# Kernel tuning notes

Hardware: AMD Instinct MI355X
Metric: run time of the kernel (lower is better)

## Reference

```python
import jax, jax.numpy as jnp
import numpy as np


def setup_inputs() -> dict:
    key = jax.random.key(0)
    ks = jax.random.split(key, 9)
    bs, F, T, d_in, Nh, d_out = 4, 8, 256, 64, 8, 64
    std = 2.0  # gaussian_init_delta_std
    return {
        "X": jax.random.normal(ks[0], (bs, F, T, d_in), dtype=jnp.float32),
        "attention_center": std * jax.random.normal(ks[1], (F, Nh, 1), dtype=jnp.float32),
        "alpha": jax.random.normal(ks[2], (F,), dtype=jnp.float32),
        "W_query": jax.random.normal(ks[3], (F, T, d_in, Nh, 2), dtype=jnp.float32),
        "W_key": jax.random.normal(ks[4], (F, T, d_in, Nh, 2), dtype=jnp.float32),
        "Wkey_": jax.random.normal(ks[5], (F, 2, 2), dtype=jnp.float32),
        "u": jax.random.normal(ks[6], (F, T, 2), dtype=jnp.float32),
        "W": jax.random.normal(ks[7], (F, Nh * d_in, d_out), dtype=jnp.float32),
        "b": jax.random.normal(ks[8], (F, T, d_out), dtype=jnp.float32),
    }


def reference(X, attention_center, alpha, W_query, W_key, Wkey_, u, W, b):
    bs, F, T, d_in = X.shape
    Nh = W_query.shape[3]

    # relative-position features R[t,l] = (l-t)^2, (l-t); identical across F in the original
    rel = (jnp.arange(T)[None, :] - jnp.arange(T)[:, None]).astype(jnp.float32)
    R = jnp.stack([rel ** 2, rel], axis=-1)  # (T,T,2)

    query = jnp.einsum('bftd,ftdhe->bfthe', X, W_query)  # (bs,F,T,Nh,2)
    key = jnp.einsum('bftd,ftdhe->bfthe', X, W_key)      # (bs,F,T,Nh,2)

    r_delta = jnp.einsum('fde,tle->ftld', Wkey_, R)      # (F,T,T,2)

    centers = jnp.concatenate([jnp.ones_like(attention_center), -2.0 * attention_center], axis=-1)  # (F,Nh,2)
    v = -alpha[:, None, None] * centers                  # (F,Nh,2)

    scores = (
        jnp.einsum('bfthe,bflhe->bfthl', query, key)
        + jnp.einsum('bfthe,ftle->bfthl', query, r_delta)
        + jnp.einsum('fle,bfthe->bfthl', u, key)
        + jnp.einsum('fhe,ftle->fthl', v, r_delta)[None]
    )  # (bs,F,T,Nh,T)

    probs = jax.nn.softmax(scores, axis=-1)

    vals = jnp.einsum('bfthl,bfld->bfthd', probs, X)     # (bs,F,T,Nh,d_in)
    vals = vals.reshape(bs, F, T, Nh * d_in)

    return jnp.einsum('bftd,fdo->bfto', vals, W) + b     # (bs,F,T,d_out)
```

## Files before the change

kernel.cpp:

```cpp
#include <hip/hip_runtime.h>
#include <hip/hip_bf16.h>

#define BS 4
#define NF 8
#define NT 256
#define DIN 64
#define NH 8
#define DOUT 64
#define TT 4
#define MROWS 32
#define NCH 64

typedef unsigned short u16;
typedef __attribute__((ext_vector_type(8))) short short8;
typedef __attribute__((ext_vector_type(4))) float f32x4;
typedef __attribute__((ext_vector_type(4))) unsigned int u32x4;

static __device__ __forceinline__ u16 f2bf(float x) {
    __hip_bfloat16 h = __float2bfloat16(x);
    u16 r; __builtin_memcpy(&r, &h, 2); return r;
}
static __device__ __forceinline__ unsigned pk2(float a, float b) {
    return (unsigned)f2bf(a) | ((unsigned)f2bf(b) << 16);
}

__global__ __launch_bounds__(256) void prep_kernel(
    const float* __restrict__ X,
    const float* __restrict__ Wq,
    const float* __restrict__ Wk,
    const float* __restrict__ W,
    float* __restrict__ q,
    float* __restrict__ kT,
    u16* __restrict__ XT,
    u16* __restrict__ Wt)
{
    __shared__ float sm[4160];
    const int tid = threadIdx.x;
    const int bid = blockIdx.x;

    if (bid < 2048) {
        const int ft = bid;
        const int f = ft >> 8, t = ft & 255;
        float* sWt = sm;
        float* sX  = sm + 2176;

        float4 a4 = ((const float4*)(Wq + ((size_t)ft << 10)))[tid];
        float4 b4 = ((const float4*)(Wk + ((size_t)ft << 10)))[tid];
        {
            int d = tid >> 2, he = (tid & 3) << 2;
            sWt[(he + 0) * 68 + d] = a4.x;
            sWt[(he + 1) * 68 + d] = a4.y;
            sWt[(he + 2) * 68 + d] = a4.z;
            sWt[(he + 3) * 68 + d] = a4.w;
            sWt[1088 + (he + 0) * 68 + d] = b4.x;
            sWt[1088 + (he + 1) * 68 + d] = b4.y;
            sWt[1088 + (he + 2) * 68 + d] = b4.z;
            sWt[1088 + (he + 3) * 68 + d] = b4.w;
            int xb = tid >> 6, xd = tid & 63;
            sX[tid] = X[(((size_t)((xb * NF + f) * NT + t)) << 6) + xd];
        }
        __syncthreads();

        const int half  = tid & 1;
        const int he    = (tid >> 1) & 15;
        const int b     = (tid >> 5) & 3;
        const int which = tid >> 7;
        const float* wp = sWt + which * 1088 + he * 68 + (half << 5);
        const float* xp = sX + (b << 6) + (half << 5);
        float acc = 0.f;
        #pragma unroll
        for (int j = 0; j < 8; ++j) {
            float4 w = *(const float4*)(wp + (j << 2));
            float4 x = *(const float4*)(xp + (j << 2));
            acc = fmaf(w.x, x.x, acc);
            acc = fmaf(w.y, x.y, acc);
            acc = fmaf(w.z, x.z, acc);
            acc = fmaf(w.w, x.w, acc);
        }
        acc += __shfl_xor(acc, 1);
        if (half == 0) {
            int bf = b * NF + f;
            if (which) kT[(((size_t)(bf * 16 + he)) << 8) + t] = acc;
            else       q[(((size_t)(bf * NT + t)) << 4) + he] = acc;
        }
    } else if (bid < 2176) {
        const int idx = bid - 2048;
        const int bf = idx >> 2, lc = idx & 3;
        float (*sT)[65] = (float(*)[65])sm;
        #pragma unroll
        for (int i = 0; i < 16; ++i) {
            int l = i * 4 + (tid >> 6), d = tid & 63;
            sT[l][d] = X[(((size_t)(bf * NT) + lc * 64 + l) << 6) + d];
        }
        __syncthreads();
        #pragma unroll
        for (int i = 0; i < 16; ++i) {
            int d = i * 4 + (tid >> 6), l = tid & 63;
            XT[(((size_t)(bf * 64) + d) << 8) + lc * 64 + l] = f2bf(sT[l][d]);
        }
    } else {
        const int idx = bid - 2176;
        const int f = idx >> 3, kc = idx & 7;
        float (*sT)[65] = (float(*)[65])sm;
        #pragma unroll
        for (int i = 0; i < 16; ++i) {
            int kk = i * 4 + (tid >> 6), o = tid & 63;
            sT[kk][o] = W[(((size_t)(f * 512) + kc * 64 + kk) << 6) + o];
        }
        __syncthreads();
        #pragma unroll
        for (int i = 0; i < 16; ++i) {
            int o = i * 4 + (tid >> 6), kk = tid & 63;
            Wt[(((size_t)(f * 64) + o) << 9) + kc * 64 + kk] = f2bf(sT[kk][o]);
        }
    }
}

__global__ __launch_bounds__(256, 4) void attn_kernel(
    const float* __restrict__ ac,
    const float* __restrict__ alpha,
    const float* __restrict__ Wkey_,
    const float* __restrict__ u,
    const float* __restrict__ bias,
    const float* __restrict__ q,
    const float* __restrict__ kT,
    const u16* __restrict__ XT,
    const u16* __restrict__ Wt,
    float* __restrict__ out)
{
    __shared__ __align__(16) u16 sPV[8320];
    __shared__ float sRed[MROWS * 16];
    __shared__ float sM[MROWS];
    __shared__ float sInvS[MROWS];

    const int tid = threadIdx.x;
    const int bid = blockIdx.x;
    const int ch = bid & 63;
    const int f  = (bid >> 6) & 7;
    const int b  = bid >> 9;
    const int bf = b * NF + f;
    const int t0 = ch * TT;

    const int h  = tid & 7;
    const int tp = (tid >> 3) & 1;
    const int lg = tid >> 4;
    const int t_a = t0 + tp * 2, t_b = t_a + 1;
    const int m_a = tp * 16 + h, m_b = m_a + 8;
    const int lbase = lg * 16;

    const float* kT0 = kT + ((size_t)bf << 12) + ((h * 2) << 8);
    const float* kT1 = kT0 + 256;
    const float* up  = u + (f << 9);

    float q0a, q1a, kt0a, kt1a, c2a, c1a;
    float q0b, q1b, kt0b, kt1b, c2b, c1b;
    {
        float al = alpha[f];
        float acv = ac[f * 8 + h];
        float wk0 = Wkey_[f * 4],     wk1 = Wkey_[f * 4 + 1];
        float wk2 = Wkey_[f * 4 + 2], wk3 = Wkey_[f * 4 + 3];
        float2 qa = *(const float2*)(q + ((size_t)(bf * NT + t_a) << 4) + (h << 1));
        float2 qb = *(const float2*)(q + ((size_t)(bf * NT + t_b) << 4) + (h << 1));
        q0a = qa.x; q1a = qa.y; q0b = qb.x; q1b = qb.y;
        kt0a = kT0[t_a]; kt1a = kT1[t_a];
        kt0b = kT0[t_b]; kt1b = kT1[t_b];
        float a0 = q0a - al, a1 = q1a + 2.f * al * acv;
        c2a = a0 * wk0 + a1 * wk2; c1a = a0 * wk1 + a1 * wk3;
        a0 = q0b - al; a1 = q1b + 2.f * al * acv;
        c2b = a0 * wk0 + a1 * wk2; c1b = a0 * wk1 + a1 * wk3;
    }

    float sA[16], sB[16];
    float mxa = -1e30f, mxb = -1e30f;
    #pragma unroll
    for (int g = 0; g < 4; ++g) {
        const int l0 = lbase + g * 4;
        float4 K0 = *(const float4*)(kT0 + l0);
        float4 K1 = *(const float4*)(kT1 + l0);
        float4 U0 = *(const float4*)(up + (l0 << 1));
        float4 U1 = *(const float4*)(up + (l0 << 1) + 4);
        float k0s[4] = {K0.x, K0.y, K0.z, K0.w};
        float k1s[4] = {K1.x, K1.y, K1.z, K1.w};
        float u0s[4] = {U0.x, U0.z, U1.x, U1.z};
        float u1s[4] = {U0.y, U0.w, U1.y, U1.w};
        #pragma unroll
        for (int j = 0; j < 4; ++j) {
            float rela = (float)(l0 + j - t_a);
            float relb = rela - 1.f;
            float sa = (c2a * rela + c1a) * rela;
            sa = fmaf(q0a, k0s[j], sa); sa = fmaf(q1a, k1s[j], sa);
            sa = fmaf(kt0a, u0s[j], sa); sa = fmaf(kt1a, u1s[j], sa);
            float sb = (c2b * relb + c1b) * relb;
            sb = fmaf(q0b, k0s[j], sb); sb = fmaf(q1b, k1s[j], sb);
            sb = fmaf(kt0b, u0s[j], sb); sb = fmaf(kt1b, u1s[j], sb);
            sA[g * 4 + j] = sa; sB[g * 4 + j] = sb;
            mxa = fmaxf(mxa, sa); mxb = fmaxf(mxb, sb);
        }
    }
    sRed[m_a * 16 + lg] = mxa;
    sRed[m_b * 16 + lg] = mxb;
    __syncthreads();
    if (tid < MROWS) {
        const float4* r4 = (const float4*)(sRed + tid * 16);
        float4 r0 = r4[0], r1 = r4[1], r2 = r4[2], r3 = r4[3];
        float mm = fmaxf(fmaxf(fmaxf(r0.x, r0.y), fmaxf(r0.z, r0.w)),
                         fmaxf(fmaxf(r1.x, r1.y), fmaxf(r1.z, r1.w)));
        mm = fmaxf(mm, fmaxf(fmaxf(fmaxf(r2.x, r2.y), fmaxf(r2.z, r2.w)),
                             fmaxf(fmaxf(r3.x, r3.y), fmaxf(r3.z, r3.w))));
        sM[tid] = mm;
    }
    __syncthreads();

    u16* sP = sPV;
    {
        const float Ma = sM[m_a], Mb = sM[m_b];
        float suma = 0.f, sumb = 0.f;
        unsigned pka[4], pkb[4];
        float epa = 0.f, epb = 0.f;
        #pragma unroll
        for (int j = 0; j < 16; ++j) {
            float ea = __expf(sA[j] - Ma), eb = __expf(sB[j] - Mb);
            suma += ea; sumb += eb;
            if ((j & 1) == 0) { epa = ea; epb = eb; }
            else { pka[(j & 7) >> 1] = pk2(epa, ea); pkb[(j & 7) >> 1] = pk2(epb, eb); }
            if ((j & 7) == 7) {
                int chunk = lg * 2 + (j >> 3);
                int pa = chunk ^ h;
                int pb = chunk ^ (h + 8);
                *(u32x4*)&sP[m_a * 256 + pa * 8] = (u32x4){pka[0], pka[1], pka[2], pka[3]};
                *(u32x4*)&sP[m_b * 256 + pb * 8] = (u32x4){pkb[0], pkb[1], pkb[2], pkb[3]};
            }
        }
        sRed[m_a * 16 + lg] = suma;
        sRed[m_b * 16 + lg] = sumb;
    }

    const int wv   = tid >> 6;
    const int lane = tid & 63;
    const int quad = lane >> 4;
    const int ln   = lane & 15;
    const int mh   = wv & 1;
    const int nh   = wv >> 1;
    const u16* xb = XT + ((size_t)bf << 14);
    short8 nb0, nb1;
    {
        int l2 = quad * 8;
        nb0 = *(const short8*)(xb + (nh * 32 + ln) * 256 + l2);
        nb1 = *(const short8*)(xb + (nh * 32 + 16 + ln) * 256 + l2);
    }
    __syncthreads();
    if (tid < MROWS) {
        const float4* r4 = (const float4*)(sRed + tid * 16);
        float4 r0 = r4[0], r1 = r4[1], r2 = r4[2], r3 = r4[3];
        float ss = ((r0.x + r0.y) + (r0.z + r0.w)) + ((r1.x + r1.y) + (r1.z + r1.w))
                 + ((r2.x + r2.y) + (r2.z + r2.w)) + ((r3.x + r3.y) + (r3.z + r3.w));
        sInvS[tid] = 1.f / ss;
    }
    __syncthreads();

    f32x4 acc0 = {0.f, 0.f, 0.f, 0.f}, acc1 = acc0;
    #pragma unroll
    for (int ks = 0; ks < 8; ++ks) {
        short8 b0 = nb0, b1 = nb1;
        if (ks < 7) {
            int l2 = (ks + 1) * 32 + quad * 8;
            nb0 = *(const short8*)(xb + (nh * 32 + ln) * 256 + l2);
            nb1 = *(const short8*)(xb + (nh * 32 + 16 + ln) * 256 + l2);
        }
        int phys = (ks * 4 + quad) ^ ln;
        short8 a = *(const short8*)&sP[(mh * 16 + ln) * 256 + phys * 8];
        acc0 = __builtin_amdgcn_mfma_f32_16x16x32_bf16(a, b0, acc0, 0, 0, 0);
        acc1 = __builtin_amdgcn_mfma_f32_16x16x32_bf16(a, b1, acc1, 0, 0, 0);
    }
    float inv0 = sInvS[mh * 16 + quad * 4 + 0];
    float inv1 = sInvS[mh * 16 + quad * 4 + 1];
    float inv2 = sInvS[mh * 16 + quad * 4 + 2];
    float inv3 = sInvS[mh * 16 + quad * 4 + 3];
    const u16* wb = Wt + ((size_t)(f * 64 + wv * 16 + ln) << 9);
    short8 nw = *(const short8*)(wb + quad * 8);
    __syncthreads();

    u16* sVals = sPV;
    {
        float invs[4] = {inv0, inv1, inv2, inv3};
        #pragma unroll
        for (int reg = 0; reg < 4; ++reg) {
            int mg = mh * 16 + quad * 4 + reg;
            int tl = mg >> 3, hh = mg & 7;
            u16* dst = sVals + tl * 520 + hh * 64 + nh * 32 + ln;
            dst[0]  = f2bf(acc0[reg] * invs[reg]);
            dst[16] = f2bf(acc1[reg] * invs[reg]);
        }
    }
    __syncthreads();

    f32x4 oacc = {0.f, 0.f, 0.f, 0.f};
    #pragma unroll
    for (int ks = 0; ks < 16; ++ks) {
        short8 bw = nw;
        if (ks < 15) nw = *(const short8*)(wb + (ks + 1) * 32 + quad * 8);
        short8 a = *(const short8*)(sVals + ln * 520 + ks * 32 + quad * 8);
        oacc = __builtin_amdgcn_mfma_f32_16x16x32_bf16(a, bw, oacc, 0, 0, 0);
    }
    {
        int o = wv * 16 + ln;
        #pragma unroll
        for (int reg = 0; reg < 4; ++reg) {
            int tl = quad * 4 + reg;
            if (tl < TT) {
                int tg = t0 + tl;
                out[((size_t)(bf * NT + tg) << 6) + o] =
                    oacc[reg] + bias[((size_t)(f * NT + tg) << 6) + o];
            }
        }
    }
}

extern "C" void kernel_launch(void* const* d_in, const int* in_sizes, int n_in,
                              void* d_out, int out_size, void* d_ws, size_t ws_size,
                              hipStream_t stream) {
    const float* X     = (const float*)d_in[0];
    const float* ac    = (const float*)d_in[1];
    const float* alpha = (const float*)d_in[2];
    const float* Wq    = (const float*)d_in[3];
    const float* Wk    = (const float*)d_in[4];
    const float* Wkey_ = (const float*)d_in[5];
    const float* u     = (const float*)d_in[6];
    const float* W     = (const float*)d_in[7];
    const float* bb    = (const float*)d_in[8];
    float* out = (float*)d_out;

    float* qws = (float*)d_ws;
    float* kTp = qws + 131072;
    u16* XT = (u16*)(kTp + 131072);
    u16* Wt = XT + 524288;

    hipLaunchKernelGGL(prep_kernel, dim3(2240), dim3(256), 0, stream,
                       X, Wq, Wk, W, qws, kTp, XT, Wt);
    hipLaunchKernelGGL(attn_kernel, dim3(BS * NF * NCH), dim3(256), 0, stream,
                       ac, alpha, Wkey_, u, bb, qws, kTp, XT, Wt, out);
}
```

Before: 125.5 us.

## Use wave-local shuffle softmax reductions instead of shared-memory block reductions

Remaps the score computation so each wavefront owns one query time step, with each lane covering 32 keys for one head. The row max and sum are then reduced with cross-lane shuffles instead of shared-memory staging, which removes three block-wide barriers and the sRed/sM arrays. The XT prefetch for the first MFMA step is also issued earlier, before the score computation. In exchange, each thread holds 32 score registers, which may raise register pressure under the launch bound.

```diff
diff --git a/kernel.cpp b/kernel.cpp
--- a/kernel.cpp
+++ b/kernel.cpp
@@ -129,8 +129,6 @@
     float* __restrict__ out)
 {
     __shared__ __align__(16) u16 sPV[8320];
-    __shared__ float sRed[MROWS * 16];
-    __shared__ float sM[MROWS];
     __shared__ float sInvS[MROWS];
 
     const int tid = threadIdx.x;
@@ -141,121 +139,93 @@
     const int bf = b * NF + f;
     const int t0 = ch * TT;
 
-    const int h  = tid & 7;
-    const int tp = (tid >> 3) & 1;
-    const int lg = tid >> 4;
-    const int t_a = t0 + tp * 2, t_b = t_a + 1;
-    const int m_a = tp * 16 + h, m_b = m_a + 8;
-    const int lbase = lg * 16;
+    const int w    = tid >> 6;
+    const int lane = tid & 63;
+    const int h    = lane & 7;
+    const int lg   = lane >> 3;
+    const int t    = t0 + w;
+    const int m    = w * 8 + h;
+    const int l0   = lg * 32;
+
+    const int quad = lane >> 4;
+    const int ln   = lane & 15;
+    const int mh   = w & 1;
+    const int nh2  = w >> 1;
+
+    const u16* xb = XT + ((size_t)bf << 14);
+    short8 nb0 = *(const short8*)(xb + (nh2 * 32 + ln) * 256 + quad * 8);
+    short8 nb1 = *(const short8*)(xb + (nh2 * 32 + 16 + ln) * 256 + quad * 8);
 
     const float* kT0 = kT + ((size_t)bf << 12) + ((h * 2) << 8);
     const float* kT1 = kT0 + 256;
     const float* up  = u + (f << 9);
 
-    float q0a, q1a, kt0a, kt1a, c2a, c1a;
-    float q0b, q1b, kt0b, kt1b, c2b, c1b;
+    float q0, q1, kt0, kt1, c2, c1;
     {
         float al = alpha[f];
         float acv = ac[f * 8 + h];
         float wk0 = Wkey_[f * 4],     wk1 = Wkey_[f * 4 + 1];
         float wk2 = Wkey_[f * 4 + 2], wk3 = Wkey_[f * 4 + 3];
-        float2 qa = *(const float2*)(q + ((size_t)(bf * NT + t_a) << 4) + (h << 1));
-        float2 qb = *(const float2*)(q + ((size_t)(bf * NT + t_b) << 4) + (h << 1));
-        q0a = qa.x; q1a = qa.y; q0b = qb.x; q1b = qb.y;
-        kt0a = kT0[t_a]; kt1a = kT1[t_a];
-        kt0b = kT0[t_b]; kt1b = kT1[t_b];
-        float a0 = q0a - al, a1 = q1a + 2.f * al * acv;
-        c2a = a0 * wk0 + a1 * wk2; c1a = a0 * wk1 + a1 * wk3;
-        a0 = q0b - al; a1 = q1b + 2.f * al * acv;
-        c2b = a0 * wk0 + a1 * wk2; c1b = a0 * wk1 + a1 * wk3;
-    }
-
-    float sA[16], sB[16];
-    float mxa = -1e30f, mxb = -1e30f;
+        float2 qv = *(const float2*)(q + ((size_t)(bf * NT + t) << 4) + (h << 1));
+        q0 = qv.x; q1 = qv.y;
+        kt0 = kT0[t]; kt1 = kT1[t];
+        float a0 = q0 - al, a1 = q1 + 2.f * al * acv;
+        c2 = a0 * wk0 + a1 * wk2; c1 = a0 * wk1 + a1 * wk3;
+    }
+
+    float s[32];
+    float mx = -1e30f;
     #pragma unroll
     for (int g = 0; g < 4; ++g) {
-        const int l0 = lbase + g * 4;
-        float4 K0 = *(const float4*)(kT0 + l0);
-        float4 K1 = *(const float4*)(kT1 + l0);
-        float4 U0 = *(const float4*)(up + (l0 << 1));
-        float4 U1 = *(const float4*)(up + (l0 << 1) + 4);
-        float k0s[4] = {K0.x, K0.y, K0.z, K0.w};
-        float k1s[4] = {K1.x, K1.y, K1.z, K1.w};
-        float u0s[4] = {U0.x, U0.z, U1.x, U1.z};
-        float u1s[4] = {U0.y, U0.w, U1.y, U1.w};
-        #pragma unroll
-        for (int j = 0; j < 4; ++j) {
-            float rela = (float)(l0 + j - t_a);
-            float relb = rela - 1.f;
-            float sa = (c2a * rela + c1a) * rela;
-            sa = fmaf(q0a, k0s[j], sa); sa = fmaf(q1a, k1s[j], sa);
-            sa = fmaf(kt0a, u0s[j], sa); sa = fmaf(kt1a, u1s[j], sa);
-            float sb = (c2b * relb + c1b) * relb;
-            sb = fmaf(q0b, k0s[j], sb); sb = fmaf(q1b, k1s[j], sb);
-            sb = fmaf(kt0b, u0s[j], sb); sb = fmaf(kt1b, u1s[j], sb);
-            sA[g * 4 + j] = sa; sB[g * 4 + j] = sb;
-            mxa = fmaxf(mxa, sa); mxb = fmaxf(mxb, sb);
-        }
-    }
-    sRed[m_a * 16 + lg] = mxa;
-    sRed[m_b * 16 + lg] = mxb;
-    __syncthreads();
-    if (tid < MROWS) {
-        const float4* r4 = (const float4*)(sRed + tid * 16);
-        float4 r0 = r4[0], r1 = r4[1], r2 = r4[2], r3 = r4[3];
-        float mm = fmaxf(fmaxf(fmaxf(r0.x, r0.y), fmaxf(r0.z, r0.w)),
-                         fmaxf(fmaxf(r1.x, r1.y), fmaxf(r1.z, r1.w)));
-        mm = fmaxf(mm, fmaxf(fmaxf(fmaxf(r2.x, r2.y), fmaxf(r2.z, r2.w)),
-                             fmaxf(fmaxf(r3.x, r3.y), fmaxf(r3.z, r3.w))));
-        sM[tid] = mm;
-    }
-    __syncthreads();
+        const int lb = l0 + g * 8;
+        float4 K0a = *(const float4*)(kT0 + lb);
+        float4 K0b = *(const float4*)(kT0 + lb + 4);
+        float4 K1a = *(const float4*)(kT1 + lb);
+        float4 K1b = *(const float4*)(kT1 + lb + 4);
+        float4 Ua = *(const float4*)(up + (lb << 1));
+        float4 Ub = *(const float4*)(up + (lb << 1) + 4);
+        float4 Uc = *(const float4*)(up + (lb << 1) + 8);
+        float4 Ud = *(const float4*)(up + (lb << 1) + 12);
+        float k0[8] = {K0a.x, K0a.y, K0a.z, K0a.w, K0b.x, K0b.y, K0b.z, K0b.w};
+        float k1[8] = {K1a.x, K1a.y, K1a.z, K1a.w, K1b.x, K1b.y, K1b.z, K1b.w};
+        float u0[8] = {Ua.x, Ua.z, Ub.x, Ub.z, Uc.x, Uc.z, Ud.x, Ud.z};
+        float u1[8] = {Ua.y, Ua.w, Ub.y, Ub.w, Uc.y, Uc.w, Ud.y, Ud.w};
+        #pragma unroll
+        for (int j = 0; j < 8; ++j) {
+            float rel = (float)(lb + j - t);
+            float sv = (c2 * rel + c1) * rel;
+            sv = fmaf(q0, k0[j], sv);
+            sv = fmaf(q1, k1[j], sv);
+            sv = fmaf(kt0, u0[j], sv);
+            sv = fmaf(kt1, u1[j], sv);
+            s[g * 8 + j] = sv;
+            mx = fmaxf(mx, sv);
+        }
+    }
+    mx = fmaxf(mx, __shfl_xor(mx, 8));
+    mx = fmaxf(mx, __shfl_xor(mx, 16));
+    mx = fmaxf(mx, __shfl_xor(mx, 32));
 
     u16* sP = sPV;
-    {
-        const float Ma = sM[m_a], Mb = sM[m_b];
-        float suma = 0.f, sumb = 0.f;
-        unsigned pka[4], pkb[4];
-        float epa = 0.f, epb = 0.f;
-        #pragma unroll
-        for (int j = 0; j < 16; ++j) {
-            float ea = __expf(sA[j] - Ma), eb = __expf(sB[j] - Mb);
-            suma += ea; sumb += eb;
-            if ((j & 1) == 0) { epa = ea; epb = eb; }
-            else { pka[(j & 7) >> 1] = pk2(epa, ea); pkb[(j & 7) >> 1] = pk2(epb, eb); }
-            if ((j & 7) == 7) {
-                int chunk = lg * 2 + (j >> 3);
-                int pa = chunk ^ h;
-                int pb = chunk ^ (h + 8);
-                *(u32x4*)&sP[m_a * 256 + pa * 8] = (u32x4){pka[0], pka[1], pka[2], pka[3]};
-                *(u32x4*)&sP[m_b * 256 + pb * 8] = (u32x4){pkb[0], pkb[1], pkb[2], pkb[3]};
-            }
-        }
-        sRed[m_a * 16 + lg] = suma;
-        sRed[m_b * 16 + lg] = sumb;
-    }
-
-    const int wv   = tid >> 6;
-    const int lane = tid & 63;
-    const int quad = lane >> 4;
-    const int ln   = lane & 15;
-    const int mh   = wv & 1;
-    const int nh   = wv >> 1;
-    const u16* xb = XT + ((size_t)bf << 14);
-    short8 nb0, nb1;
-    {
-        int l2 = quad * 8;
-        nb0 = *(const short8*)(xb + (nh * 32 + ln) * 256 + l2);
-        nb1 = *(const short8*)(xb + (nh * 32 + 16 + ln) * 256 + l2);
-    }
-    __syncthreads();
-    if (tid < MROWS) {
-        const float4* r4 = (const float4*)(sRed + tid * 16);
-        float4 r0 = r4[0], r1 = r4[1], r2 = r4[2], r3 = r4[3];
-        float ss = ((r0.x + r0.y) + (r0.z + r0.w)) + ((r1.x + r1.y) + (r1.z + r1.w))
-                 + ((r2.x + r2.y) + (r2.z + r2.w)) + ((r3.x + r3.y) + (r3.z + r3.w));
-        sInvS[tid] = 1.f / ss;
-    }
+    float sum = 0.f;
+    #pragma unroll
+    for (int c = 0; c < 4; ++c) {
+        unsigned pk4[4];
+        #pragma unroll
+        for (int jj = 0; jj < 8; jj += 2) {
+            float e0 = __expf(s[c * 8 + jj] - mx);
+            float e1 = __expf(s[c * 8 + jj + 1] - mx);
+            sum += e0 + e1;
+            pk4[jj >> 1] = pk2(e0, e1);
+        }
+        int chunk = lg * 4 + c;
+        int phys = chunk ^ (m & 15);
+        *(u32x4*)&sP[m * 256 + phys * 8] = (u32x4){pk4[0], pk4[1], pk4[2], pk4[3]};
+    }
+    sum += __shfl_xor(sum, 8);
+    sum += __shfl_xor(sum, 16);
+    sum += __shfl_xor(sum, 32);
+    if (lg == 0) sInvS[m] = 1.f / sum;
     __syncthreads();
 
     f32x4 acc0 = {0.f, 0.f, 0.f, 0.f}, acc1 = acc0;
@@ -264,8 +234,8 @@
         short8 b0 = nb0, b1 = nb1;
         if (ks < 7) {
             int l2 = (ks + 1) * 32 + quad * 8;
-            nb0 = *(const short8*)(xb + (nh * 32 + ln) * 256 + l2);
-            nb1 = *(const short8*)(xb + (nh * 32 + 16 + ln) * 256 + l2);
+            nb0 = *(const short8*)(xb + (nh2 * 32 + ln) * 256 + l2);
+            nb1 = *(const short8*)(xb + (nh2 * 32 + 16 + ln) * 256 + l2);
         }
         int phys = (ks * 4 + quad) ^ ln;
         short8 a = *(const short8*)&sP[(mh * 16 + ln) * 256 + phys * 8];
@@ -276,7 +246,7 @@
     float inv1 = sInvS[mh * 16 + quad * 4 + 1];
     float inv2 = sInvS[mh * 16 + quad * 4 + 2];
     float inv3 = sInvS[mh * 16 + quad * 4 + 3];
-    const u16* wb = Wt + ((size_t)(f * 64 + wv * 16 + ln) << 9);
+    const u16* wb = Wt + ((size_t)(f * 64 + w * 16 + ln) << 9);
     short8 nw = *(const short8*)(wb + quad * 8);
     __syncthreads();
 
@@ -287,7 +257,7 @@
         for (int reg = 0; reg < 4; ++reg) {
             int mg = mh * 16 + quad * 4 + reg;
             int tl = mg >> 3, hh = mg & 7;
-            u16* dst = sVals + tl * 520 + hh * 64 + nh * 32 + ln;
+            u16* dst = sVals + tl * 520 + hh * 64 + nh2 * 32 + ln;
             dst[0]  = f2bf(acc0[reg] * invs[reg]);
             dst[16] = f2bf(acc1[reg] * invs[reg]);
         }
@@ -303,7 +273,7 @@
         oacc = __builtin_amdgcn_mfma_f32_16x16x32_bf16(a, bw, oacc, 0, 0, 0);
     }
     {
-        int o = wv * 16 + ln;
+        int o = w * 16 + ln;
         #pragma unroll
         for (int reg = 0; reg < 4; ++reg) {
             int tl = quad * 4 + reg;
```

After: 139.4 us. 11.1% more time.
